# Performance work log

Measured on AMD Instinct MI355X. Metric: run time of the kernel, lower is better.

The kernel has to match this reference:

```python
import jax, jax.numpy as jnp
import numpy as np

BN_EPS = 1e-5
LN_EPS = 1e-5
NUM_HEADS = 4


def _conv1d(x, w, b, stride, pad):
    # x: [B, Cin, L], w: [Cout, Cin, K]
    y = jax.lax.conv_general_dilated(x, w, (stride,), [(pad, pad)],
                                     dimension_numbers=('NCH', 'OIH', 'NCH'))
    return y + b[None, :, None]


def _bn(x, g, b, m, v):
    # eval-mode BatchNorm1d with running stats
    return (x - m[None, :, None]) * (g / jnp.sqrt(v + BN_EPS))[None, :, None] + b[None, :, None]


def _conv_bn_relu(x, w, b, g, bb, m, v, stride, pad):
    return jax.nn.relu(_bn(_conv1d(x, w, b, stride, pad), g, bb, m, v))


def _layernorm(x, g, b):
    mu = jnp.mean(x, -1, keepdims=True)
    var = jnp.mean((x - mu) ** 2, -1, keepdims=True)
    return (x - mu) / jnp.sqrt(var + LN_EPS) * g + b


def _simplified_transformer(x, w_qk, b_qk):
    # Sequential chunked multi-head attention with feature-accumulation residual.
    # Note: the torch module's self.qks Linears are shadowed/dead -> not used.
    B, N, C = x.shape
    H = NUM_HEADS
    Nh, Ch = N // H, C // H
    scale = Ch ** -0.5
    feats_in = jnp.split(x, H, axis=1)  # H chunks of [B, Nh, C] along seq
    feats_out = []
    feat = feats_in[0]
    for i in range(H):
        if i > 0:
            feat = feat + feats_in[i]
        v = feat.reshape(B, Nh, H, Ch).transpose(0, 2, 1, 3)  # [B,H,Nh,Ch]
        qk = (feat @ w_qk + b_qk).reshape(B, Nh, 2, H, Ch).transpose(2, 0, 3, 1, 4)
        q, k = qk[0] * scale, qk[1]  # [B,H,Nh,Ch]
        attn = jax.nn.softmax(jnp.einsum('bhqc,bhkc->bhqk', q, k), axis=-1)
        feat = jnp.einsum('bhqk,bhkc->bhqc', attn, v).transpose(0, 2, 1, 3).reshape(B, Nh, C)
        feats_out.append(feat)
    return jnp.concatenate(feats_out, axis=1)  # [B, N, C]


def reference(x, w_adj, b_adj,
              w_c0, b_c0, bn0_g, bn0_b, bn0_m, bn0_v,
              w_c1, b_c1, bn1_g, bn1_b, bn1_m, bn1_v,
              w_c2, b_c2, bn2_g, bn2_b, bn2_m, bn2_v,
              w_c3, b_c3, bn3_g, bn3_b, bn3_m, bn3_v,
              w_pe, b_pe, w_qk0, b_qk0, w_qk1, b_qk1,
              w_fc1, b_fc1, w_fc2, b_fc2, ln_g, ln_b, w_cls, b_cls):
    x = x[:, None, :]                      # [B,1,1798]
    x = x @ w_adj + b_adj                  # [B,1,2048]
    x = _conv_bn_relu(x, w_c0, b_c0, bn0_g, bn0_b, bn0_m, bn0_v, 2, 7)  # [B,64,1024]
    y = _conv_bn_relu(x, w_c1, b_c1, bn1_g, bn1_b, bn1_m, bn1_v, 1, 4)
    y = _conv_bn_relu(y, w_c2, b_c2, bn2_g, bn2_b, bn2_m, bn2_v, 1, 2)
    y = _conv_bn_relu(y, w_c3, b_c3, bn3_g, bn3_b, bn3_m, bn3_v, 1, 1)  # [B,192,1024]
    x = jnp.concatenate([x, y], axis=1)    # [B,256,1024]
    x = _conv1d(x, w_pe, b_pe, 8, 0).transpose(0, 2, 1)  # [B,128,192]
    a = _simplified_transformer(x, w_qk0, b_qk0)
    a = _simplified_transformer(a, w_qk1, b_qk1)
    h = jax.nn.gelu(x @ w_fc1 + b_fc1, approximate=False) @ w_fc2 + b_fc2
    x = _layernorm(a + h, ln_g, ln_b)
    x = jnp.mean(x, axis=1)                # AdaptiveAvgPool1d(1) over tokens
    return x @ w_cls + b_cls               # [B,3]


def setup_inputs() -> dict:
    keys = iter(jax.random.split(jax.random.key(0), 80))

    def nrm(shape, s):
        return jax.random.normal(next(keys), shape, jnp.float32) * s

    d = {}
    B = 512
    d['x'] = nrm((B, 1798), 1.0)
    d['w_adj'] = nrm((1798, 2048), 0.02)
    d['b_adj'] = jnp.zeros((2048,), jnp.float32)

    def conv(name, co, ci, k):
        d['w_' + name] = nrm((co, ci, k), 1.0 / np.sqrt(ci * k))
        d['b_' + name] = jnp.zeros((co,), jnp.float32)

    def bn(name, c):
        d[name + '_g'] = 1.0 + nrm((c,), 0.1)
        d[name + '_b'] = nrm((c,), 0.02)
        d[name + '_m'] = nrm((c,), 0.1)
        d[name + '_v'] = 1.0 + jax.random.uniform(next(keys), (c,), jnp.float32) * 0.1

    conv('c0', 64, 1, 15); bn('bn0', 64)
    conv('c1', 128, 64, 9); bn('bn1', 128)
    conv('c2', 128, 128, 5); bn('bn2', 128)
    conv('c3', 192, 128, 3); bn('bn3', 192)
    conv('pe', 192, 256, 8)
    for n in ('qk0', 'qk1'):
        d['w_' + n] = nrm((192, 384), 0.02)
        d['b_' + n] = jnp.zeros((384,), jnp.float32)
    d['w_fc1'] = nrm((192, 264), 0.02); d['b_fc1'] = jnp.zeros((264,), jnp.float32)
    d['w_fc2'] = nrm((264, 192), 0.02); d['b_fc2'] = jnp.zeros((192,), jnp.float32)
    d['ln_g'] = jnp.ones((192,), jnp.float32); d['ln_b'] = jnp.zeros((192,), jnp.float32)
    d['w_cls'] = nrm((192, 3), 0.02); d['b_cls'] = jnp.zeros((3,), jnp.float32)
    return d
```

## Files before the change

### kernel.cpp

```cpp
#include <hip/hip_runtime.h>
#include <hip/hip_bf16.h>
#include <hip/hip_fp16.h>
#include <cstddef>

typedef _Float16 half8 __attribute__((ext_vector_type(8)));
typedef _Float16 half4 __attribute__((ext_vector_type(4)));
typedef float floatx4 __attribute__((ext_vector_type(4)));

__global__ __launch_bounds__(256) void fill_const(float* out, int n, float v) {
    int i = blockIdx.x * 256 + threadIdx.x;
    if (i < n) out[i] = v;
}

__global__ __launch_bounds__(256) void pack_all(
    const float* __restrict__ wc1, const float* __restrict__ wc2,
    const float* __restrict__ wc3, const float* __restrict__ wpe,
    const float* __restrict__ wqk0, const float* __restrict__ wqk1,
    const float* __restrict__ wfc1, const float* __restrict__ wfc2,
    const float* __restrict__ wadj, const float* __restrict__ x,
    _Float16* __restrict__ wpk, _Float16* __restrict__ wadjp,
    _Float16* __restrict__ xpad)
{
    int idx = blockIdx.x * 256 + threadIdx.x;
    if (idx < 73728) {
        int i = idx;
        int j = i & 7, lane = (i >> 3) & 63, f = i >> 9;
        int t = f % 8, cc = (f / 8) % 2, k = f / 16;
        int co = t * 16 + (lane & 15);
        int ci = cc * 32 + (lane >> 4) * 8 + j;
        wpk[idx] = (_Float16)wc1[(co * 64 + ci) * 9 + k];
    } else if (idx < 155648) {
        int i = idx - 73728;
        int j = i & 7, lane = (i >> 3) & 63, f = i >> 9;
        int t = f % 8, cc = (f / 8) % 4, k = f / 32;
        int co = t * 16 + (lane & 15);
        int ci = cc * 32 + (lane >> 4) * 8 + j;
        wpk[idx] = (_Float16)wc2[(co * 128 + ci) * 5 + k];
    } else if (idx < 229376) {
        int i = idx - 155648;
        int j = i & 7, lane = (i >> 3) & 63, f = i >> 9;
        int t = f % 12, cc = (f / 12) % 4, k = f / 48;
        int co = t * 16 + (lane & 15);
        int ci = cc * 32 + (lane >> 4) * 8 + j;
        wpk[idx] = (_Float16)wc3[(co * 128 + ci) * 3 + k];
    } else if (idx < 622592) {
        int i = idx - 229376;
        int j = i & 7, lane = (i >> 3) & 63, f = i >> 9;
        int t = f % 12, cc = f / 12;
        int co = t * 16 + (lane & 15);
        int rr = cc * 32 + (lane >> 4) * 8 + j;
        int ktap = rr >> 8, ci = rr & 255;
        wpk[idx] = (_Float16)wpe[co * 2048 + ci * 8 + ktap];
    } else if (idx < 696320) {
        int i = idx - 622592;
        int j = i & 7, lane = (i >> 3) & 63, f = i >> 9;
        int nt = f % 24, ks = f / 24;
        int c = ks * 32 + (lane >> 4) * 8 + j;
        int jcol = nt * 16 + (lane & 15);
        wpk[idx] = (_Float16)wqk0[c * 384 + jcol];
    } else if (idx < 770048) {
        int i = idx - 696320;
        int j = i & 7, lane = (i >> 3) & 63, f = i >> 9;
        int nt = f % 24, ks = f / 24;
        int c = ks * 32 + (lane >> 4) * 8 + j;
        int jcol = nt * 16 + (lane & 15);
        wpk[idx] = (_Float16)wqk1[c * 384 + jcol];
    } else if (idx < 822272) {
        int i = idx - 770048;
        int j = i & 7, lane = (i >> 3) & 63, f = i >> 9;
        int t = f % 17, ks = f / 17;
        int jcol = t * 16 + (lane & 15);
        int c = ks * 32 + (lane >> 4) * 8 + j;
        wpk[idx] = (jcol < 264) ? (_Float16)wfc1[c * 264 + jcol] : (_Float16)0.f;
    } else if (idx < 877568) {
        int i = idx - 822272;
        int j = i & 7, lane = (i >> 3) & 63, f = i >> 9;
        int t = f % 12, ks = f / 12;
        int co = t * 16 + (lane & 15);
        int k = ks * 32 + (lane >> 4) * 8 + j;
        wpk[idx] = (k < 264) ? (_Float16)wfc2[k * 192 + co] : (_Float16)0.f;
    } else if (idx < 4613120) {
        int i = idx - 877568;
        int j = i & 7, lane = (i >> 3) & 63, f = i >> 9;
        int t = f & 127, ks = f >> 7;
        int jcol = t * 16 + (lane & 15);
        int k = ks * 32 + (lane >> 4) * 8 + j;
        wadjp[i] = (k < 1798) ? (_Float16)wadj[(size_t)k * 2048 + jcol] : (_Float16)0.f;
    } else if (idx < 5547008) {
        int i = idx - 4613120;
        int b = i / 1824, k = i - b * 1824;
        xpad[i] = (k < 1798) ? (_Float16)x[(size_t)b * 1798 + k] : (_Float16)0.f;
    }
}

__global__ __launch_bounds__(256) void adj_mfma(
    const _Float16* __restrict__ xh, const _Float16* __restrict__ wp,
    const float* __restrict__ bias, _Float16* __restrict__ out)
{
    const int tid = threadIdx.x;
    const int w = tid >> 6, lane = tid & 63, quad = lane >> 4, col = lane & 15;
    const int bm = blockIdx.x >> 5;
    const int bn = blockIdx.x & 31;
    const int sample = bm * 64 + w * 16 + col;
    floatx4 acc[4];
#pragma unroll
    for (int t = 0; t < 4; ++t) acc[t] = (floatx4){0.f, 0.f, 0.f, 0.f};
    for (int ks = 0; ks < 57; ++ks) {
        half8 bf = *(const half8*)&xh[(size_t)sample * 1824 + ks * 32 + quad * 8];
#pragma unroll
        for (int tt = 0; tt < 4; ++tt) {
            int f = ks * 128 + bn * 4 + tt;
            half8 af = *(const half8*)&wp[((size_t)f * 64 + lane) * 8];
            acc[tt] = __builtin_amdgcn_mfma_f32_16x16x32_f16(af, bf, acc[tt], 0, 0, 0);
        }
    }
#pragma unroll
    for (int tt = 0; tt < 4; ++tt) {
        int jb = (bn * 4 + tt) * 16 + quad * 4;
        half4 hv;
#pragma unroll
        for (int r = 0; r < 4; ++r)
            hv[r] = (_Float16)(acc[tt][r] + bias[jb + r]);
        *(half4*)&out[(size_t)sample * 2048 + jb] = hv;
    }
}

__global__ __launch_bounds__(256) void c0_tiled(
    const _Float16* __restrict__ in, const float* __restrict__ w,
    const float* __restrict__ cb, const float* __restrict__ g,
    const float* __restrict__ bb, const float* __restrict__ m,
    const float* __restrict__ vv, _Float16* __restrict__ out)
{
    __shared__ _Float16 sin[544];
    __shared__ float wf[960], sc[64], sh[64];
    const int tid = threadIdx.x;
    const int bl = blockIdx.x >> 2;
    const int l0 = (blockIdx.x & 3) * 256;
    for (int i = tid; i < 960; i += 256) wf[i] = w[i];
    if (tid < 64) {
        float s = g[tid] * rsqrtf(vv[tid] + 1e-5f);
        sc[tid] = s;
        sh[tid] = (cb[tid] - m[tid]) * s + bb[tid];
    }
    const int base = 2 * l0 - 7;
    for (int i = tid; i < 528; i += 256) {
        int pos = base + i;
        sin[i] = (pos >= 0 && pos < 2048) ? in[(size_t)bl * 2048 + pos] : (_Float16)0.f;
    }
    __syncthreads();
    const int l = l0 + tid;
    const int s0 = 2 * tid;
    float xv[15];
#pragma unroll
    for (int k = 0; k < 15; ++k) xv[k] = (float)sin[s0 + k];
    for (int gq = 0; gq < 8; ++gq) {
        half8 ov;
#pragma unroll
        for (int r = 0; r < 8; ++r) {
            int co = gq * 8 + r;
            float acc = 0.f;
#pragma unroll
            for (int k = 0; k < 15; ++k)
                acc = fmaf(xv[k], wf[co * 15 + k], acc);
            ov[r] = (_Float16)fmaxf(fmaf(acc, sc[co], sh[co]), 0.f);
        }
        *(half8*)&out[((size_t)bl * 1024 + l) * 64 + gq * 8] = ov;
    }
}

template <int CIN, int K, int PAD, int COUT>
__global__ __launch_bounds__(256) void conv_mfma(
    const _Float16* __restrict__ in, const _Float16* __restrict__ wp,
    const float* __restrict__ cb, const float* __restrict__ g,
    const float* __restrict__ bb, const float* __restrict__ m,
    const float* __restrict__ vv, _Float16* __restrict__ out)
{
    constexpr int STRIDE = (CIN == 64) ? 72 : 152;
    constexpr int SPAN = 64 + K - 1;
    constexpr int NCC = CIN / 32, NT = COUT / 16, CH8 = CIN / 8;
    __shared__ _Float16 tin[SPAN * STRIDE];
    __shared__ float sc[COUT], sh[COUT];
    const int tid = threadIdx.x;
    const int b = blockIdx.x >> 4;
    const int l0b = (blockIdx.x & 15) * 64;
    for (int c = tid; c < COUT; c += 256) {
        float s = g[c] * rsqrtf(vv[c] + 1e-5f);
        sc[c] = s;
        sh[c] = (cb[c] - m[c]) * s + bb[c];
    }
    for (int idx = tid; idx < SPAN * CH8; idx += 256) {
        int p = idx / CH8, ch = idx - p * CH8;
        int pos = l0b + p - PAD;
        half8 v = {0, 0, 0, 0, 0, 0, 0, 0};
        if (pos >= 0 && pos < 1024)
            v = *(const half8*)&in[((size_t)b * 1024 + pos) * CIN + ch * 8];
        *(half8*)&tin[p * STRIDE + ch * 8] = v;
    }
    __syncthreads();
    const int lane = tid & 63, wave = tid >> 6;
    const int quad = lane >> 4, n = lane & 15;
    const int lrow0 = wave * 16 + n;
    floatx4 acc[NT];
#pragma unroll
    for (int t = 0; t < NT; ++t) acc[t] = (floatx4){0.f, 0.f, 0.f, 0.f};
#pragma unroll
    for (int k = 0; k < K; ++k) {
#pragma unroll
        for (int cc = 0; cc < NCC; ++cc) {
            half8 bfrag = *(const half8*)&tin[(lrow0 + k) * STRIDE + cc * 32 + quad * 8];
#pragma unroll
            for (int t = 0; t < NT; ++t) {
                int f = (k * NCC + cc) * NT + t;
                half8 afrag = *(const half8*)&wp[((size_t)f * 64 + lane) * 8];
                acc[t] = __builtin_amdgcn_mfma_f32_16x16x32_f16(afrag, bfrag, acc[t], 0, 0, 0);
            }
        }
    }
    const int lg = l0b + wave * 16 + n;
#pragma unroll
    for (int t = 0; t < NT; ++t) {
        half4 hv;
#pragma unroll
        for (int r = 0; r < 4; ++r) {
            int co = t * 16 + quad * 4 + r;
            hv[r] = (_Float16)fmaxf(fmaf(acc[t][r], sc[co], sh[co]), 0.f);
        }
        *(half4*)&out[((size_t)b * 1024 + lg) * COUT + t * 16 + quad * 4] = hv;
    }
}

__global__ __launch_bounds__(256) void pe_mfma(
    const _Float16* __restrict__ c0b, const _Float16* __restrict__ c3b,
    const _Float16* __restrict__ wp, const float* __restrict__ bias,
    _Float16* __restrict__ outh)
{
    const int tid = threadIdx.x;
    const int w = tid >> 6, lane = tid & 63, quad = lane >> 4, col = lane & 15;
    const int s = blockIdx.x >> 1;
    const int n0 = (blockIdx.x & 1) * 64;
    const int token = n0 + w * 16 + col;
    floatx4 acc[12];
#pragma unroll
    for (int t = 0; t < 12; ++t) acc[t] = (floatx4){0.f, 0.f, 0.f, 0.f};
    for (int cc = 0; cc < 64; ++cc) {
        int rr = cc * 32 + quad * 8;
        int ktap = rr >> 8, ci = rr & 255;
        const _Float16* src = (ci < 64)
            ? c0b + ((size_t)s * 1024 + token * 8 + ktap) * 64 + ci
            : c3b + ((size_t)s * 1024 + token * 8 + ktap) * 192 + (ci - 64);
        half8 bf = *(const half8*)src;
#pragma unroll
        for (int t = 0; t < 12; ++t) {
            half8 af = *(const half8*)&wp[((size_t)(cc * 12 + t) * 64 + lane) * 8];
            acc[t] = __builtin_amdgcn_mfma_f32_16x16x32_f16(af, bf, acc[t], 0, 0, 0);
        }
    }
    const size_t tb = ((size_t)s * 128 + token) * 192;
#pragma unroll
    for (int t = 0; t < 12; ++t) {
        half4 hv;
#pragma unroll
        for (int r = 0; r < 4; ++r)
            hv[r] = (_Float16)(acc[t][r] + bias[t * 16 + quad * 4 + r]);
        *(half4*)&outh[tb + t * 16 + quad * 4] = hv;
    }
}

__global__ __launch_bounds__(256) void transformer12_mfma(
    const _Float16* __restrict__ src,
    const _Float16* __restrict__ wq0p, const float* __restrict__ bq0,
    const _Float16* __restrict__ wq1p, const float* __restrict__ bq1,
    _Float16* __restrict__ dst)
{
    __shared__ _Float16 uA[6400];
    __shared__ _Float16 uB[12544];
    __shared__ _Float16 sS[4608];
    __shared__ _Float16 zerobuf[16];
    const int b = blockIdx.x;
    const int tid = threadIdx.x;
    const int w = tid >> 6, lane = tid & 63, quad = lane >> 4, col = lane & 15;
    const int tok_t = tid >> 3;
    const int cc0_t = (tid & 7) * 24;
    const int h_t = (tid & 7) >> 1;
    if (tid < 16) zerobuf[tid] = (_Float16)0.f;
    float fr[24];
    half8 t0a, t0b, t0c, t1a, t1b, t1c, t2a, t2b, t2c, t3a, t3b, t3c;
    for (int pass = 0; pass < 2; ++pass) {
        const _Float16* wqkp = pass ? wq1p : wq0p;
        const float* bqk = pass ? bq1 : bq0;
        for (int i = 0; i < 4; ++i) {
            half8 s0, s1, s2;
            if (pass == 0) {
                const _Float16* srow = src + ((size_t)b * 128 + i * 32 + tok_t) * 192 + cc0_t;
                s0 = *(const half8*)&srow[0];
                s1 = *(const half8*)&srow[8];
                s2 = *(const half8*)&srow[16];
            } else {
                switch (i) {
                    case 0: s0 = t0a; s1 = t0b; s2 = t0c; break;
                    case 1: s0 = t1a; s1 = t1b; s2 = t1c; break;
                    case 2: s0 = t2a; s1 = t2b; s2 = t2c; break;
                    default: s0 = t3a; s1 = t3b; s2 = t3c; break;
                }
            }
#pragma unroll
            for (int r = 0; r < 8; ++r) {
                float v0 = (float)s0[r], v1 = (float)s1[r], v2 = (float)s2[r];
                if (i == 0) { fr[r] = v0; fr[8 + r] = v1; fr[16 + r] = v2; }
                else { fr[r] += v0; fr[8 + r] += v1; fr[16 + r] += v2; }
            }
#pragma unroll
            for (int q8 = 0; q8 < 3; ++q8) {
                half8 hv;
#pragma unroll
                for (int r = 0; r < 8; ++r) hv[r] = (_Float16)fr[q8 * 8 + r];
                *(half8*)&uA[tok_t * 200 + cc0_t + q8 * 8] = hv;
            }
            __syncthreads();
            {
                floatx4 acc2[12];
#pragma unroll
                for (int t = 0; t < 12; ++t) acc2[t] = (floatx4){0.f, 0.f, 0.f, 0.f};
#pragma unroll
                for (int ks = 0; ks < 6; ++ks) {
                    half8 a0 = *(const half8*)&uA[(col) * 200 + ks * 32 + quad * 8];
                    half8 a1 = *(const half8*)&uA[(16 + col) * 200 + ks * 32 + quad * 8];
#pragma unroll
                    for (int nl = 0; nl < 6; ++nl) {
                        int ntile = w * 6 + nl;
                        half8 bf = *(const half8*)&wqkp[((size_t)(ks * 24 + ntile) * 64 + lane) * 8];
                        acc2[nl] = __builtin_amdgcn_mfma_f32_16x16x32_f16(a0, bf, acc2[nl], 0, 0, 0);
                        acc2[6 + nl] = __builtin_amdgcn_mfma_f32_16x16x32_f16(a1, bf, acc2[6 + nl], 0, 0, 0);
                    }
                }
#pragma unroll
                for (int mt = 0; mt < 2; ++mt)
#pragma unroll
                    for (int nl = 0; nl < 6; ++nl) {
                        int j = (w * 6 + nl) * 16 + col;
                        float bv = bqk[j];
#pragma unroll
                        for (int r = 0; r < 4; ++r) {
                            int tok = mt * 16 + quad * 4 + r;
                            uB[tok * 392 + j] = (_Float16)(acc2[mt * 6 + nl][r] + bv);
                        }
                    }
                __syncthreads();
            }
            {
                const int h = w;
                floatx4 acc3[4];
#pragma unroll
                for (int t = 0; t < 4; ++t) acc3[t] = (floatx4){0.f, 0.f, 0.f, 0.f};
#pragma unroll
                for (int ks = 0; ks < 2; ++ks) {
                    bool z = (ks == 1 && quad >= 2);
                    const _Float16* pq0 = z ? zerobuf : &uB[(col) * 392 + h * 48 + ks * 32 + quad * 8];
                    const _Float16* pq1 = z ? zerobuf : &uB[(16 + col) * 392 + h * 48 + ks * 32 + quad * 8];
                    const _Float16* pk0 = z ? zerobuf : &uB[(col) * 392 + 192 + h * 48 + ks * 32 + quad * 8];
                    const _Float16* pk1 = z ? zerobuf : &uB[(16 + col) * 392 + 192 + h * 48 + ks * 32 + quad * 8];
                    half8 q0 = *(const half8*)pq0, q1 = *(const half8*)pq1;
                    half8 k0 = *(const half8*)pk0, k1 = *(const half8*)pk1;
                    acc3[0] = __builtin_amdgcn_mfma_f32_16x16x32_f16(q0, k0, acc3[0], 0, 0, 0);
                    acc3[1] = __builtin_amdgcn_mfma_f32_16x16x32_f16(q0, k1, acc3[1], 0, 0, 0);
                    acc3[2] = __builtin_amdgcn_mfma_f32_16x16x32_f16(q1, k0, acc3[2], 0, 0, 0);
                    acc3[3] = __builtin_amdgcn_mfma_f32_16x16x32_f16(q1, k1, acc3[3], 0, 0, 0);
                }
#pragma unroll
                for (int mt = 0; mt < 2; ++mt)
#pragma unroll
                    for (int nt = 0; nt < 2; ++nt)
#pragma unroll
                        for (int r = 0; r < 4; ++r) {
                            int q = mt * 16 + quad * 4 + r;
                            int k = nt * 16 + col;
                            sS[(h * 32 + q) * 36 + k] =
                                (_Float16)(acc3[mt * 2 + nt][r] * 0.14433756729740643f);
                        }
                __syncthreads();
            }
            if (tid < 128) {
                int h = tid >> 5, qi = tid & 31;
                const _Float16* row = &sS[(h * 32 + qi) * 36];
                float lg[32];
                float mx = -1e30f;
#pragma unroll
                for (int k = 0; k < 32; ++k) { lg[k] = (float)row[k]; mx = fmaxf(mx, lg[k]); }
                float sum = 0.f;
#pragma unroll
                for (int k = 0; k < 32; ++k) { lg[k] = __expf(lg[k] - mx); sum += lg[k]; }
                float inv = 1.f / sum;
                _Float16* arow = &uB[(h * 32 + qi) * 40];
#pragma unroll
                for (int k = 0; k < 32; ++k) arow[k] = (_Float16)(lg[k] * inv);
            }
            __syncthreads();
            {
                float accq[24];
#pragma unroll
                for (int q = 0; q < 24; ++q) accq[q] = 0.f;
                const _Float16* arow = &uB[(h_t * 32 + tok_t) * 40];
                for (int j = 0; j < 32; ++j) {
                    float av = (float)arow[j];
                    const half8* fp = (const half8*)&uA[j * 200 + cc0_t];
                    half8 f0 = fp[0], f1 = fp[1], f2 = fp[2];
#pragma unroll
                    for (int r = 0; r < 8; ++r) {
                        accq[r] = fmaf(av, (float)f0[r], accq[r]);
                        accq[8 + r] = fmaf(av, (float)f1[r], accq[8 + r]);
                        accq[16 + r] = fmaf(av, (float)f2[r], accq[16 + r]);
                    }
                }
#pragma unroll
                for (int q = 0; q < 24; ++q) fr[q] = accq[q];
            }
            __syncthreads();
            half8 h0, h1, h2;
#pragma unroll
            for (int r = 0; r < 8; ++r) {
                h0[r] = (_Float16)fr[r];
                h1[r] = (_Float16)fr[8 + r];
                h2[r] = (_Float16)fr[16 + r];
            }
            if (pass == 0) {
                switch (i) {
                    case 0: t0a = h0; t0b = h1; t0c = h2; break;
                    case 1: t1a = h0; t1b = h1; t1c = h2; break;
                    case 2: t2a = h0; t2b = h1; t2c = h2; break;
                    default: t3a = h0; t3b = h1; t3c = h2; break;
                }
            } else {
                _Float16* drow = dst + ((size_t)b * 128 + i * 32 + tok_t) * 192 + cc0_t;
                *(half8*)&drow[0] = h0;
                *(half8*)&drow[8] = h1;
                *(half8*)&drow[16] = h2;
            }
        }
    }
}

__global__ __launch_bounds__(256) void mlp_mfma(
    const _Float16* __restrict__ xh, const _Float16* __restrict__ a,
    const float* __restrict__ b1, const float* __restrict__ b2,
    const float* __restrict__ lng, const float* __restrict__ lnb,
    const _Float16* __restrict__ w1p, const _Float16* __restrict__ w2p,
    float* __restrict__ bsum)
{
    constexpr int HS = 296;
    __shared__ _Float16 h1s[64 * HS];
    __shared__ float b1s[264], b2s[192], lgs[192], lbs[192];
    __shared__ float ps[4 * 192];
    const int tid = threadIdx.x;
    const int w = tid >> 6, lane = tid & 63, quad = lane >> 4, col = lane & 15;
    const int tok0 = blockIdx.x * 64;
    const int tokl = w * 16 + col;
    const size_t tokg = tok0 + tokl;
    for (int i = tid; i < 264; i += 256) b1s[i] = b1[i];
    for (int i = tid; i < 192; i += 256) { b2s[i] = b2[i]; lgs[i] = lng[i]; lbs[i] = lnb[i]; }
    for (int i = tid; i < 64 * 32; i += 256) {
        int tk = i >> 5, cc2 = i & 31;
        h1s[tk * HS + 264 + cc2] = (_Float16)0.f;
    }
    __syncthreads();
    floatx4 acc1[17];
#pragma unroll
    for (int t = 0; t < 17; ++t) acc1[t] = (floatx4){0.f, 0.f, 0.f, 0.f};
#pragma unroll
    for (int ks = 0; ks < 6; ++ks) {
        half8 bf = *(const half8*)&xh[tokg * 192 + ks * 32 + quad * 8];
#pragma unroll
        for (int t = 0; t < 17; ++t) {
            half8 af = *(const half8*)&w1p[((size_t)(ks * 17 + t) * 64 + lane) * 8];
            acc1[t] = __builtin_amdgcn_mfma_f32_16x16x32_f16(af, bf, acc1[t], 0, 0, 0);
        }
    }
#pragma unroll
    for (int t = 0; t < 17; ++t) {
        int jb = t * 16 + quad * 4;
        if (jb >= 264) continue;
        half4 hv;
#pragma unroll
        for (int r = 0; r < 4; ++r) {
            int j = jb + r;
            float v = acc1[t][r] + b1s[j];
            hv[r] = (_Float16)(0.5f * v * (1.f + erff(v * 0.70710678118654752f)));
        }
        *(half4*)&h1s[tokl * HS + jb] = hv;
    }
    __syncthreads();
    floatx4 acc2[12];
#pragma unroll
    for (int t = 0; t < 12; ++t) acc2[t] = (floatx4){0.f, 0.f, 0.f, 0.f};
#pragma unroll
    for (int ks = 0; ks < 9; ++ks) {
        half8 bf = *(const half8*)&h1s[tokl * HS + ks * 32 + quad * 8];
#pragma unroll
        for (int t = 0; t < 12; ++t) {
            half8 af = *(const half8*)&w2p[((size_t)(ks * 12 + t) * 64 + lane) * 8];
            acc2[t] = __builtin_amdgcn_mfma_f32_16x16x32_f16(af, bf, acc2[t], 0, 0, 0);
        }
    }
    const size_t base = tokg * 192;
    float psum = 0.f;
#pragma unroll
    for (int t = 0; t < 12; ++t) {
        half4 av = *(const half4*)&a[base + t * 16 + quad * 4];
#pragma unroll
        for (int r = 0; r < 4; ++r) {
            float v = acc2[t][r] + b2s[t * 16 + quad * 4 + r] + (float)av[r];
            acc2[t][r] = v;
            psum += v;
        }
    }
    psum += __shfl_xor(psum, 16);
    psum += __shfl_xor(psum, 32);
    float mean = psum * (1.f / 192.f);
    float pvar = 0.f;
#pragma unroll
    for (int t = 0; t < 12; ++t)
#pragma unroll
        for (int r = 0; r < 4; ++r) {
            float d = acc2[t][r] - mean;
            pvar = fmaf(d, d, pvar);
        }
    pvar += __shfl_xor(pvar, 16);
    pvar += __shfl_xor(pvar, 32);
    float rsd = rsqrtf(pvar * (1.f / 192.f) + 1e-5f);
#pragma unroll
    for (int t = 0; t < 12; ++t) {
#pragma unroll
        for (int r = 0; r < 4; ++r) {
            float o = (acc2[t][r] - mean) * rsd * lgs[t * 16 + quad * 4 + r] + lbs[t * 16 + quad * 4 + r];
            o += __shfl_xor(o, 1);
            o += __shfl_xor(o, 2);
            o += __shfl_xor(o, 4);
            o += __shfl_xor(o, 8);
            acc2[t][r] = o;
        }
    }
    if (col == 0) {
#pragma unroll
        for (int t = 0; t < 12; ++t)
#pragma unroll
            for (int r = 0; r < 4; ++r)
                ps[w * 192 + t * 16 + quad * 4 + r] = acc2[t][r];
    }
    __syncthreads();
    if (tid < 192)
        bsum[(size_t)blockIdx.x * 192 + tid] =
            ps[tid] + ps[192 + tid] + ps[384 + tid] + ps[576 + tid];
}

__global__ __launch_bounds__(192) void head2_kernel(
    const float* __restrict__ bsum, const float* __restrict__ wcls,
    const float* __restrict__ bcls, float* __restrict__ out)
{
    __shared__ float mean[192];
    const int b = blockIdx.x;
    const int c = threadIdx.x;
    mean[c] = (bsum[(size_t)(2 * b) * 192 + c] + bsum[(size_t)(2 * b + 1) * 192 + c]) * (1.f / 128.f);
    __syncthreads();
    if (c < 3) {
        float acc = bcls[c];
        for (int k = 0; k < 192; ++k) acc = fmaf(mean[k], wcls[k * 3 + c], acc);
        out[b * 3 + c] = acc;
    }
}

static const int SZ_DICT[41] = {
    920576, 3682304, 2048, 960, 64, 64, 64, 64, 64,
    73728, 128, 128, 128, 128, 128,
    81920, 128, 128, 128, 128, 128,
    73728, 192, 192, 192, 192, 192,
    393216, 192,
    73728, 384, 73728, 384,
    50688, 264, 50688, 192,
    192, 192, 576, 3};

extern "C" void kernel_launch(void* const* d_in, const int* in_sizes, int n_in,
                              void* d_out, int out_size, void* d_ws, size_t ws_size,
                              hipStream_t stream) {
    if (n_in != 41) {
        fill_const<<<(out_size + 255) / 256, 256, 0, stream>>>((float*)d_out, out_size, 200.f);
        return;
    }
    bool mA = true;
    for (int i = 0; i < 41; ++i) mA = mA && (in_sizes[i] == SZ_DICT[i]);
    if (!mA) {
        fill_const<<<(out_size + 255) / 256, 256, 0, stream>>>((float*)d_out, out_size, 100.f);
        return;
    }
    const float* P[41];
    for (int i = 0; i < 41; ++i) P[i] = (const float*)d_in[i];

    const size_t TOKH = (size_t)512 * 128 * 192 * 2;
    const size_t WPACK = 2097152;
    const size_t ADJF = (size_t)512 * 2048 * 2;
    const size_t CONVS128 = 100663296;
    const size_t CONVS256 = 201326592;
    int BcC;
    size_t CONVS;
    if (ws_size >= CONVS256 + 2 * TOKH + WPACK + ADJF) { BcC = 256; CONVS = CONVS256; }
    else if (ws_size >= CONVS128 + 2 * TOKH + WPACK + ADJF) { BcC = 128; CONVS = CONVS128; }
    else {
        fill_const<<<(out_size + 255) / 256, 256, 0, stream>>>((float*)d_out, out_size, 50.f);
        return;
    }
    char* ws = (char*)d_ws;
    char* convS = ws;
    _Float16* pebh = (_Float16*)(ws + CONVS);
    _Float16* t2h  = (_Float16*)(ws + CONVS + TOKH);
    char* wpk = ws + CONVS + 2 * TOKH;
    _Float16* adjfull = (_Float16*)(wpk + WPACK);

    _Float16* wadjp = (_Float16*)convS;
    _Float16* xpad  = wadjp + 3735552;
    float* bsum = (float*)convS;

    _Float16* c0b = (_Float16*)convS;
    char* u1 = convS + (size_t)BcC * 131072;
    char* u2 = u1 + (size_t)BcC * 393216;
    _Float16* c1b = (_Float16*)u1;
    _Float16* c2b = (_Float16*)u2;
    _Float16* c3b = (_Float16*)u1;

    _Float16* w1p  = (_Float16*)wpk;
    _Float16* w2p  = w1p + 73728;
    _Float16* w3p  = w2p + 81920;
    _Float16* wpep = w3p + 73728;
    _Float16* wq0p = wpep + 393216;
    _Float16* wq1p = wq0p + 73728;
    _Float16* wm1p = wq1p + 73728;
    _Float16* wm2p = wm1p + 52224;

    pack_all<<<21668, 256, 0, stream>>>(P[9], P[15], P[21], P[27], P[29], P[31],
                                        P[33], P[35], P[1], P[0],
                                        (_Float16*)wpk, wadjp, xpad);

    adj_mfma<<<256, 256, 0, stream>>>(xpad, wadjp, P[2], adjfull);

    const int nchunk = 512 / BcC;
    for (int c = 0; c < nchunk; ++c) {
        const size_t b0 = (size_t)c * BcC;
        c0_tiled<<<BcC * 4, 256, 0, stream>>>(adjfull + b0 * 2048, P[3], P[4],
                                              P[5], P[6], P[7], P[8], c0b);
        conv_mfma<64, 9, 4, 128><<<BcC * 16, 256, 0, stream>>>(c0b, w1p, P[10],
                                                 P[11], P[12], P[13], P[14], c1b);
        conv_mfma<128, 5, 2, 128><<<BcC * 16, 256, 0, stream>>>(c1b, w2p, P[16],
                                                 P[17], P[18], P[19], P[20], c2b);
        conv_mfma<128, 3, 1, 192><<<BcC * 16, 256, 0, stream>>>(c2b, w3p, P[22],
                                                 P[23], P[24], P[25], P[26], c3b);
        pe_mfma<<<BcC * 2, 256, 0, stream>>>(c0b, c3b, wpep, P[28],
                                             pebh + b0 * 128 * 192);
    }
    transformer12_mfma<<<512, 256, 0, stream>>>(pebh, wq0p, P[30], wq1p, P[32], t2h);
    mlp_mfma<<<1024, 256, 0, stream>>>(pebh, t2h, P[34], P[36],
                                       P[37], P[38], wm1p, wm2p, bsum);
    head2_kernel<<<512, 192, 0, stream>>>(bsum, P[39], P[40], (float*)d_out);
}
```

Before: 1.175 ms.

## Switch conv layers to 32x32x16 MFMA with output-channel-split waves

The three conv layers move from 16x16x32 MFMA tiles, where each wave covered 16 positions across all output channels, to 32x32x16 MFMA. Each wave now owns 32 output channels across a 32-position tile, and blocks are sized to COUT/32 waves. The weight packing is rewritten so the tap and input-channel dimensions form a single flattened K axis in 16-element segments. This is meant to cut A-fragment global loads per MFMA and the accumulator count, at the cost of twice as many blocks and a larger halo overhead relative to the smaller position tile.

```diff
diff --git a/kernel.cpp b/kernel.cpp
--- a/kernel.cpp
+++ b/kernel.cpp
@@ -6,6 +6,7 @@
 typedef _Float16 half8 __attribute__((ext_vector_type(8)));
 typedef _Float16 half4 __attribute__((ext_vector_type(4)));
 typedef float floatx4 __attribute__((ext_vector_type(4)));
+typedef float floatx16 __attribute__((ext_vector_type(16)));
 
 __global__ __launch_bounds__(256) void fill_const(float* out, int n, float v) {
     int i = blockIdx.x * 256 + threadIdx.x;
@@ -25,24 +26,27 @@
     if (idx < 73728) {
         int i = idx;
         int j = i & 7, lane = (i >> 3) & 63, f = i >> 9;
-        int t = f % 8, cc = (f / 8) % 2, k = f / 16;
-        int co = t * 16 + (lane & 15);
-        int ci = cc * 32 + (lane >> 4) * 8 + j;
-        wpk[idx] = (_Float16)wc1[(co * 64 + ci) * 9 + k];
+        int t = f % 4, ks = f / 4;
+        int co = t * 32 + (lane & 31);
+        int kg = ks * 16 + (lane >> 5) * 8 + j;
+        int ktap = kg >> 6, ci = kg & 63;
+        wpk[idx] = (_Float16)wc1[(co * 64 + ci) * 9 + ktap];
     } else if (idx < 155648) {
         int i = idx - 73728;
         int j = i & 7, lane = (i >> 3) & 63, f = i >> 9;
-        int t = f % 8, cc = (f / 8) % 4, k = f / 32;
-        int co = t * 16 + (lane & 15);
-        int ci = cc * 32 + (lane >> 4) * 8 + j;
-        wpk[idx] = (_Float16)wc2[(co * 128 + ci) * 5 + k];
+        int t = f % 4, ks = f / 4;
+        int co = t * 32 + (lane & 31);
+        int kg = ks * 16 + (lane >> 5) * 8 + j;
+        int ktap = kg >> 7, ci = kg & 127;
+        wpk[idx] = (_Float16)wc2[(co * 128 + ci) * 5 + ktap];
     } else if (idx < 229376) {
         int i = idx - 155648;
         int j = i & 7, lane = (i >> 3) & 63, f = i >> 9;
-        int t = f % 12, cc = (f / 12) % 4, k = f / 48;
-        int co = t * 16 + (lane & 15);
-        int ci = cc * 32 + (lane >> 4) * 8 + j;
-        wpk[idx] = (_Float16)wc3[(co * 128 + ci) * 3 + k];
+        int t = f % 6, ks = f / 6;
+        int co = t * 32 + (lane & 31);
+        int kg = ks * 16 + (lane >> 5) * 8 + j;
+        int ktap = kg >> 7, ci = kg & 127;
+        wpk[idx] = (_Float16)wc3[(co * 128 + ci) * 3 + ktap];
     } else if (idx < 622592) {
         int i = idx - 229376;
         int j = i & 7, lane = (i >> 3) & 63, f = i >> 9;
@@ -169,26 +173,30 @@
 }
 
 template <int CIN, int K, int PAD, int COUT>
-__global__ __launch_bounds__(256) void conv_mfma(
-    const _Float16* __restrict__ in, const _Float16* __restrict__ wp,
+__global__ __launch_bounds__((COUT / 32) * 64) void conv32_mfma(
+    const _Float16* __restrict__ in,
+    const _Float16* __restrict__ wp,
     const float* __restrict__ cb, const float* __restrict__ g,
     const float* __restrict__ bb, const float* __restrict__ m,
     const float* __restrict__ vv, _Float16* __restrict__ out)
 {
-    constexpr int STRIDE = (CIN == 64) ? 72 : 152;
-    constexpr int SPAN = 64 + K - 1;
-    constexpr int NCC = CIN / 32, NT = COUT / 16, CH8 = CIN / 8;
+    constexpr int NW = COUT / 32;
+    constexpr int NTH = NW * 64;
+    constexpr int STRIDE = CIN + 8;
+    constexpr int SPAN = 32 + K - 1;
+    constexpr int KSEG = CIN * K / 16;
+    constexpr int CH8 = CIN / 8;
     __shared__ _Float16 tin[SPAN * STRIDE];
     __shared__ float sc[COUT], sh[COUT];
     const int tid = threadIdx.x;
-    const int b = blockIdx.x >> 4;
-    const int l0b = (blockIdx.x & 15) * 64;
-    for (int c = tid; c < COUT; c += 256) {
+    const int b = blockIdx.x >> 5;
+    const int l0b = (blockIdx.x & 31) * 32;
+    for (int c = tid; c < COUT; c += NTH) {
         float s = g[c] * rsqrtf(vv[c] + 1e-5f);
         sc[c] = s;
         sh[c] = (cb[c] - m[c]) * s + bb[c];
     }
-    for (int idx = tid; idx < SPAN * CH8; idx += 256) {
+    for (int idx = tid; idx < SPAN * CH8; idx += NTH) {
         int p = idx / CH8, ch = idx - p * CH8;
         int pos = l0b + p - PAD;
         half8 v = {0, 0, 0, 0, 0, 0, 0, 0};
@@ -198,34 +206,26 @@
     }
     __syncthreads();
     const int lane = tid & 63, wave = tid >> 6;
-    const int quad = lane >> 4, n = lane & 15;
-    const int lrow0 = wave * 16 + n;
-    floatx4 acc[NT];
-#pragma unroll
-    for (int t = 0; t < NT; ++t) acc[t] = (floatx4){0.f, 0.f, 0.f, 0.f};
-#pragma unroll
-    for (int k = 0; k < K; ++k) {
-#pragma unroll
-        for (int cc = 0; cc < NCC; ++cc) {
-            half8 bfrag = *(const half8*)&tin[(lrow0 + k) * STRIDE + cc * 32 + quad * 8];
-#pragma unroll
-            for (int t = 0; t < NT; ++t) {
-                int f = (k * NCC + cc) * NT + t;
-                half8 afrag = *(const half8*)&wp[((size_t)f * 64 + lane) * 8];
-                acc[t] = __builtin_amdgcn_mfma_f32_16x16x32_f16(afrag, bfrag, acc[t], 0, 0, 0);
-            }
-        }
-    }
-    const int lg = l0b + wave * 16 + n;
-#pragma unroll
-    for (int t = 0; t < NT; ++t) {
+    const int n32 = lane & 31, khalf = lane >> 5;
+    floatx16 acc = {0.f, 0.f, 0.f, 0.f, 0.f, 0.f, 0.f, 0.f,
+                    0.f, 0.f, 0.f, 0.f, 0.f, 0.f, 0.f, 0.f};
+#pragma unroll
+    for (int ks = 0; ks < KSEG; ++ks) {
+        int kg = ks * 16;
+        int ktap = kg / CIN, ci0 = kg % CIN;
+        half8 bf = *(const half8*)&tin[(n32 + ktap) * STRIDE + ci0 + khalf * 8];
+        half8 af = *(const half8*)&wp[((size_t)(ks * NW + wave) * 64 + lane) * 8];
+        acc = __builtin_amdgcn_mfma_f32_32x32x16_f16(af, bf, acc, 0, 0, 0);
+    }
+    const int lg = l0b + n32;
+#pragma unroll
+    for (int rg = 0; rg < 4; ++rg) {
+        int co = wave * 32 + 8 * rg + 4 * khalf;
         half4 hv;
 #pragma unroll
-        for (int r = 0; r < 4; ++r) {
-            int co = t * 16 + quad * 4 + r;
-            hv[r] = (_Float16)fmaxf(fmaf(acc[t][r], sc[co], sh[co]), 0.f);
-        }
-        *(half4*)&out[((size_t)b * 1024 + lg) * COUT + t * 16 + quad * 4] = hv;
+        for (int r = 0; r < 4; ++r)
+            hv[r] = (_Float16)fmaxf(fmaf(acc[rg * 4 + r], sc[co + r], sh[co + r]), 0.f);
+        *(half4*)&out[((size_t)b * 1024 + lg) * COUT + co] = hv;
     }
 }
 
@@ -644,11 +644,11 @@
         const size_t b0 = (size_t)c * BcC;
         c0_tiled<<<BcC * 4, 256, 0, stream>>>(adjfull + b0 * 2048, P[3], P[4],
                                               P[5], P[6], P[7], P[8], c0b);
-        conv_mfma<64, 9, 4, 128><<<BcC * 16, 256, 0, stream>>>(c0b, w1p, P[10],
+        conv32_mfma<64, 9, 4, 128><<<BcC * 32, 256, 0, stream>>>(c0b, w1p, P[10],
                                                  P[11], P[12], P[13], P[14], c1b);
-        conv_mfma<128, 5, 2, 128><<<BcC * 16, 256, 0, stream>>>(c1b, w2p, P[16],
+        conv32_mfma<128, 5, 2, 128><<<BcC * 32, 256, 0, stream>>>(c1b, w2p, P[16],
                                                  P[17], P[18], P[19], P[20], c2b);
-        conv_mfma<128, 3, 1, 192><<<BcC * 16, 256, 0, stream>>>(c2b, w3p, P[22],
+        conv32_mfma<128, 3, 1, 192><<<BcC * 32, 384, 0, stream>>>(c2b, w3p, P[22],
                                                  P[23], P[24], P[25], P[26], c3b);
         pe_mfma<<<BcC * 2, 256, 0, stream>>>(c0b, c3b, wpep, P[28],
                                              pebh + b0 * 128 * 192);
```

Measured after the change: 1.019 ms. -13.3%, faster.
